# Kernel optimization log

Hardware: AMD Instinct MI355X
Metric: run time of the kernel (lower is better)

The kernel has to match this reference:

```python
import jax, jax.numpy as jnp
import numpy as np

EMBED_DIM = 1024


def setup_inputs() -> dict:
    key = jax.random.key(0)
    ks = jax.random.split(key, 8)
    B, S, D = 4, 2048, EMBED_DIM
    scale = 1.0 / np.sqrt(D)
    x = jax.random.normal(ks[0], (B, S, D), dtype=jnp.float32)
    mask = jnp.zeros((S, S), dtype=jnp.float32)
    # nn.Linear default init ~ U(-1/sqrt(fan_in), 1/sqrt(fan_in)); exact dist irrelevant for correctness
    w_q = jax.random.uniform(ks[1], (D, D), jnp.float32, -scale, scale)
    b_q = jax.random.uniform(ks[2], (D,), jnp.float32, -scale, scale)
    w_k = jax.random.uniform(ks[3], (D, D), jnp.float32, -scale, scale)
    b_k = jax.random.uniform(ks[4], (D,), jnp.float32, -scale, scale)
    w_v = jax.random.uniform(ks[5], (D, D), jnp.float32, -scale, scale)
    b_v = jax.random.uniform(ks[6], (D,), jnp.float32, -scale, scale)
    return {"x": x, "mask": mask, "w_q": w_q, "b_q": b_q,
            "w_k": w_k, "b_k": b_k, "w_v": w_v, "b_v": b_v}


def reference(x, mask, w_q, b_q, w_k, b_k, w_v, b_v):
    D = x.shape[-1]
    # nn.Linear computes x @ W^T + b
    Q = jnp.einsum('bsd,ed->bse', x, w_q) + b_q
    K = jnp.einsum('bsd,ed->bse', x, w_k) + b_k
    V = jnp.einsum('bsd,ed->bse', x, w_v) + b_v
    scores = jnp.einsum('bqd,bkd->bqk', Q, K) / jnp.sqrt(jnp.asarray(D, x.dtype))
    scores = scores + mask  # additive mask, broadcast over batch
    attn = jax.nn.softmax(scores, axis=-1)
    return jnp.einsum('bqk,bkd->bqd', attn, V)
```

## Files before the change

### kernel.cpp

```cpp
#include <hip/hip_runtime.h>


typedef __attribute__((ext_vector_type(8))) short short8;
typedef __attribute__((ext_vector_type(4))) short short4v;
typedef __attribute__((ext_vector_type(4))) float float4v;

__device__ __forceinline__ short f2bf(float f) {
  unsigned u = __builtin_bit_cast(unsigned, f);
  u += 0x7fffu + ((u >> 16) & 1u);
  return (short)(u >> 16);
}
__device__ __forceinline__ float bf2f(short s) {
  unsigned u = ((unsigned)(unsigned short)s) << 16;
  return __builtin_bit_cast(float, u);
}

__device__ __forceinline__ void gl2lds16(const void* g, void* l) {
  __builtin_amdgcn_global_load_lds((const __attribute__((address_space(1))) void*)g,
                                   (__attribute__((address_space(3))) void*)l, 16, 0, 0);
}

__global__ __launch_bounds__(256) void prep_kernel(const float* __restrict__ x,
                                                   const float* __restrict__ wq,
                                                   const float* __restrict__ wk,
                                                   const float* __restrict__ wv,
                                                   const float* __restrict__ bq,
                                                   const float* __restrict__ bk,
                                                   short* __restrict__ x_bf,
                                                   short* __restrict__ w_bf,
                                                   float* __restrict__ bcat) {
  int b = blockIdx.x;
  if (b < 3072) {
    int seg = b >> 10;
    const float* w = seg == 0 ? wq : (seg == 1 ? wk : wv);
    int i = (b - (seg << 10)) * 256 + threadIdx.x;
    float4v v = ((const float4v*)w)[i];
    short4v o;
    o.x = f2bf(v.x); o.y = f2bf(v.y); o.z = f2bf(v.z); o.w = f2bf(v.w);
    ((short4v*)(w_bf + (long)seg * 1048576))[i] = o;
  } else if (b < 11264) {
    int i = (b - 3072) * 256 + threadIdx.x;
    float4v v = ((const float4v*)x)[i];
    short4v o;
    o.x = f2bf(v.x); o.y = f2bf(v.y); o.z = f2bf(v.z); o.w = f2bf(v.w);
    ((short4v*)x_bf)[i] = o;
  } else {
    int i = (b - 11264) * 256 + threadIdx.x;
    if (i < 2048) bcat[i] = i < 1024 ? bq[i] : bk[i - 1024];
  }
}

__device__ __forceinline__ void stage_half(const short* __restrict__ g, int ld,
                                           int grow0, int kt, short* lds, int t) {
  const int r = t >> 3;
  const int cch = (t & 7) ^ (r & 7);
  const long co = (long)kt + cch * 8;
  gl2lds16(g + (long)(grow0 + r) * ld + co, lds + t * 8);
  gl2lds16(g + (long)(grow0 + 64 + r) * ld + co, lds + 4096 + t * 8);
}

template <int EPI, int MH>
__device__ __forceinline__ void gemm_body(const short* __restrict__ A,
                                          const short* __restrict__ Bm,
                                          void* __restrict__ C,
                                          const float* __restrict__ aux,
                                          float* __restrict__ rsum, float scale,
                                          int N, int Kd, int Bld, int m0, int n0,
                                          short (*As)[64], short (*Bs)[64]) {
  const int t = threadIdx.x;
  const int lane = t & 63;
  const int wave = t >> 6;
  const int wm = (wave >> 2) * 64 * MH;
  const int wn = (wave & 3) * 64;
  const int col = lane & 15, quad = lane >> 4;
  const int sw = col & 7;
  const int NT = Kd >> 6;
  constexpr int AS = 128 * MH;

  float4v acc[4 * MH][4] = {};

  stage_half(A, Kd, m0, 0, &As[0][0], t);
  if constexpr (MH == 2) stage_half(A, Kd, m0 + 128, 0, &As[128][0], t);
  stage_half(Bm, Bld, n0, 0, &Bs[0][0], t);
  stage_half(Bm, Bld, n0 + 128, 0, &Bs[128][0], t);
  if (NT > 1) {
    stage_half(A, Kd, m0, 64, &As[AS][0], t);
    if constexpr (MH == 2) stage_half(A, Kd, m0 + 128, 64, &As[AS + 128][0], t);
    stage_half(Bm, Bld, n0, 64, &Bs[256][0], t);
    stage_half(Bm, Bld, n0 + 128, 64, &Bs[384][0], t);
    if constexpr (MH == 2)
      asm volatile("s_waitcnt vmcnt(8)" ::: "memory");
    else
      asm volatile("s_waitcnt vmcnt(6)" ::: "memory");
  } else {
    asm volatile("s_waitcnt vmcnt(0)" ::: "memory");
  }
  __builtin_amdgcn_s_barrier();

  int ar = 0;
  int aw = 2 * AS;
  int br = 0;

  for (int k = 0; k < NT; ++k) {
    short8 a[4][2], b0[2][2], b1[2][2];

    if constexpr (MH == 2) {
#pragma unroll
      for (int i = 0; i < 4; ++i)
#pragma unroll
        for (int s = 0; s < 2; ++s)
          a[i][s] = *(const short8*)&As[ar + wm + i * 16 + col][(((s * 4 + quad) ^ sw)) * 8];
#pragma unroll
      for (int j = 0; j < 2; ++j)
#pragma unroll
        for (int s = 0; s < 2; ++s)
          b0[j][s] = *(const short8*)&Bs[br + wn + j * 16 + col][(((s * 4 + quad) ^ sw)) * 8];
      if (k + 2 < NT) stage_half(A, Kd, m0, (k + 2) * 64, &As[aw][0], t);
      __builtin_amdgcn_s_barrier();
      __builtin_amdgcn_s_setprio(1);
#pragma unroll
      for (int i = 0; i < 4; ++i)
#pragma unroll
        for (int j = 0; j < 2; ++j)
#pragma unroll
          for (int s = 0; s < 2; ++s)
            acc[i][j] = __builtin_amdgcn_mfma_f32_16x16x32_bf16(a[i][s], b0[j][s], acc[i][j], 0, 0, 0);
      __builtin_amdgcn_s_setprio(0);

#pragma unroll
      for (int j = 0; j < 2; ++j)
#pragma unroll
        for (int s = 0; s < 2; ++s)
          b1[j][s] = *(const short8*)&Bs[br + wn + (j + 2) * 16 + col][(((s * 4 + quad) ^ sw)) * 8];
      if (k + 2 < NT) stage_half(A, Kd, m0 + 128, (k + 2) * 64, &As[aw + 128][0], t);
      __builtin_amdgcn_s_barrier();
      __builtin_amdgcn_s_setprio(1);
#pragma unroll
      for (int i = 0; i < 4; ++i)
#pragma unroll
        for (int j = 0; j < 2; ++j)
#pragma unroll
          for (int s = 0; s < 2; ++s)
            acc[i][j + 2] = __builtin_amdgcn_mfma_f32_16x16x32_bf16(a[i][s], b1[j][s], acc[i][j + 2], 0, 0, 0);
      __builtin_amdgcn_s_setprio(0);

#pragma unroll
      for (int i = 0; i < 4; ++i)
#pragma unroll
        for (int s = 0; s < 2; ++s)
          a[i][s] = *(const short8*)&As[ar + wm + (i + 4) * 16 + col][(((s * 4 + quad) ^ sw)) * 8];
      if (k + 2 < NT) stage_half(Bm, Bld, n0, (k + 2) * 64, &Bs[br][0], t);
      __builtin_amdgcn_s_barrier();
      __builtin_amdgcn_s_setprio(1);
#pragma unroll
      for (int i = 0; i < 4; ++i)
#pragma unroll
        for (int j = 0; j < 2; ++j)
#pragma unroll
          for (int s = 0; s < 2; ++s)
            acc[i + 4][j + 2] = __builtin_amdgcn_mfma_f32_16x16x32_bf16(a[i][s], b1[j][s], acc[i + 4][j + 2], 0, 0, 0);
      __builtin_amdgcn_s_setprio(0);

      if (k + 2 < NT) stage_half(Bm, Bld, n0 + 128, (k + 2) * 64, &Bs[br + 128][0], t);
      if (k + 2 < NT) {
        asm volatile("s_waitcnt vmcnt(8)" ::: "memory");
      } else if (k + 1 < NT) {
        asm volatile("s_waitcnt vmcnt(0)" ::: "memory");
      }
      __builtin_amdgcn_s_barrier();
      __builtin_amdgcn_s_setprio(1);
#pragma unroll
      for (int i = 0; i < 4; ++i)
#pragma unroll
        for (int j = 0; j < 2; ++j)
#pragma unroll
          for (int s = 0; s < 2; ++s)
            acc[i + 4][j] = __builtin_amdgcn_mfma_f32_16x16x32_bf16(a[i][s], b0[j][s], acc[i + 4][j], 0, 0, 0);
      __builtin_amdgcn_s_setprio(0);
    } else {
#pragma unroll
      for (int i = 0; i < 4; ++i)
#pragma unroll
        for (int s = 0; s < 2; ++s)
          a[i][s] = *(const short8*)&As[ar + wm + i * 16 + col][(((s * 4 + quad) ^ sw)) * 8];
#pragma unroll
      for (int j = 0; j < 2; ++j)
#pragma unroll
        for (int s = 0; s < 2; ++s)
          b0[j][s] = *(const short8*)&Bs[br + wn + j * 16 + col][(((s * 4 + quad) ^ sw)) * 8];
      if (k + 2 < NT) stage_half(A, Kd, m0, (k + 2) * 64, &As[aw][0], t);
      __builtin_amdgcn_s_barrier();
      __builtin_amdgcn_s_setprio(1);
#pragma unroll
      for (int i = 0; i < 4; ++i)
#pragma unroll
        for (int j = 0; j < 2; ++j)
#pragma unroll
          for (int s = 0; s < 2; ++s)
            acc[i][j] = __builtin_amdgcn_mfma_f32_16x16x32_bf16(a[i][s], b0[j][s], acc[i][j], 0, 0, 0);
      __builtin_amdgcn_s_setprio(0);

#pragma unroll
      for (int j = 0; j < 2; ++j)
#pragma unroll
        for (int s = 0; s < 2; ++s)
          b1[j][s] = *(const short8*)&Bs[br + wn + (j + 2) * 16 + col][(((s * 4 + quad) ^ sw)) * 8];
      if (k + 2 < NT) {
        stage_half(Bm, Bld, n0, (k + 2) * 64, &Bs[br][0], t);
        stage_half(Bm, Bld, n0 + 128, (k + 2) * 64, &Bs[br + 128][0], t);
        asm volatile("s_waitcnt vmcnt(6)" ::: "memory");
      } else if (k + 1 < NT) {
        asm volatile("s_waitcnt vmcnt(0)" ::: "memory");
      }
      __builtin_amdgcn_s_barrier();
      __builtin_amdgcn_s_setprio(1);
#pragma unroll
      for (int i = 0; i < 4; ++i)
#pragma unroll
        for (int j = 0; j < 2; ++j)
#pragma unroll
          for (int s = 0; s < 2; ++s)
            acc[i][j + 2] = __builtin_amdgcn_mfma_f32_16x16x32_bf16(a[i][s], b1[j][s], acc[i][j + 2], 0, 0, 0);
      __builtin_amdgcn_s_setprio(0);
    }

    ar = (ar == 2 * AS) ? 0 : ar + AS;
    aw = (aw == 2 * AS) ? 0 : aw + AS;
    br ^= 256;
  }

  float* invb = (float*)&Bs[0][0];
  if (EPI == 2) {
    __syncthreads();
    if (t < 128 * MH) {
      float s = 0.f;
#pragma unroll
      for (int p = 0; p < 32; ++p) s += aux[p * 8192 + m0 + t];
      invb[t] = __builtin_amdgcn_rcpf(s);
    }
    __syncthreads();
  }

  const float LOG2E = 1.44269504f;
  const float c1 = scale * LOG2E;
#pragma unroll
  for (int i = 0; i < 4 * MH; ++i) {
    float invv[4], addm[4], rsum4[4] = {0.f, 0.f, 0.f, 0.f};
    if (EPI == 2) {
#pragma unroll
      for (int r = 0; r < 4; ++r) invv[r] = invb[wm + i * 16 + quad * 4 + r];
    }
    if (EPI == 3) {
#pragma unroll
      for (int r = 0; r < 4; ++r) addm[r] = aux[m0 + wm + i * 16 + quad * 4 + r];
    }
#pragma unroll
    for (int j = 0; j < 4; ++j) {
      const int n = n0 + wn + j * 16 + col;
      float addn = 0.f;
      if (EPI == 0) addn = aux[n];
#pragma unroll
      for (int r = 0; r < 4; ++r) {
        const int m = m0 + wm + i * 16 + quad * 4 + r;
        float v = acc[i][j][r];
        if (EPI == 0) {
          ((short*)C)[(long)m * N + n] = f2bf(v + addn);
        } else if (EPI == 1) {
          float mv = aux[(long)m * N + n];
          float e = exp2f(fmaf(v, c1, mv * LOG2E));
          short q = f2bf(e);
          ((short*)C)[(long)m * N + n] = q;
          rsum4[r] += bf2f(q);
        } else if (EPI == 2) {
          ((float*)C)[(long)m * N + n] = v * invv[r];
        } else {
          ((short*)C)[(long)m * N + n] = f2bf(v + addm[r]);
        }
      }
    }
    if (EPI == 1) {
#pragma unroll
      for (int r = 0; r < 4; ++r) {
        float s = rsum4[r];
        s += __shfl_xor(s, 1);
        s += __shfl_xor(s, 2);
        s += __shfl_xor(s, 4);
        s += __shfl_xor(s, 8);
        if (col == 0)
          rsum[(wave & 3) * 8192 + m0 + wm + i * 16 + quad * 4 + r] = s;
      }
    }
  }
}

__global__ __launch_bounds__(512, 2) void qkv_kernel(const short* __restrict__ x_bf,
                                                     const short* __restrict__ w_bf,
                                                     short* __restrict__ QK,
                                                     short* __restrict__ Vt,
                                                     const float* __restrict__ bcat,
                                                     const float* __restrict__ bv) {
  __shared__ alignas(16) short As[768][64];
  __shared__ alignas(16) short Bs[512][64];
  const int b = blockIdx.x;
  const int g = (b & 7) * 64 + (b >> 3);
  if (g < 256) {
    const int bz = g >> 7, r = g & 127;
    const int m0 = (r >> 2) * 256, n0 = (r & 3) * 256;
    gemm_body<0, 2>(x_bf, w_bf + (long)bz * 1048576, QK + (long)bz * 8388608,
                    bcat + bz * 1024, nullptr, 1.f, 1024, 1024, 1024, m0, n0, As, Bs);
  } else {
    const int v = g - 256;
    const int m0 = (v >> 5) * 128, n0 = (v & 31) * 256;
    gemm_body<3, 1>(w_bf + 2097152, x_bf, Vt, bv, nullptr, 1.f,
                    8192, 1024, 1024, m0, n0, As, Bs);
  }
}

__global__ __launch_bounds__(512, 2) void scores_kernel(const short* __restrict__ Q,
                                                        const short* __restrict__ Kb,
                                                        short* __restrict__ P,
                                                        const float* __restrict__ mask,
                                                        float* __restrict__ rspart) {
  __shared__ alignas(16) short As[768][64];
  __shared__ alignas(16) short Bs[512][64];
  const int b = blockIdx.x;
  const int g = (b & 7) * 32 + (b >> 3);
  const int bz = g >> 6, t2 = g & 63;
  const int m0 = (t2 >> 3) * 256, n0 = (t2 & 7) * 256;
  gemm_body<1, 2>(Q + (long)bz * 2097152, Kb + (long)bz * 2097152,
                  P + (long)bz * 4194304, mask,
                  rspart + (long)(n0 >> 8) * 4 * 8192 + bz * 2048, 0.03125f,
                  2048, 1024, 1024, m0, n0, As, Bs);
}

__global__ __launch_bounds__(512, 2) void pv_kernel(const short* __restrict__ P,
                                                    const short* __restrict__ Vt,
                                                    float* __restrict__ out,
                                                    const float* __restrict__ rspart) {
  __shared__ alignas(16) short As[384][64];
  __shared__ alignas(16) short Bs[512][64];
  const int b = blockIdx.x;
  const int g = (b & 7) * 32 + (b >> 3);
  const int bz = g >> 6, t2 = g & 63;
  const int m0 = (t2 >> 2) * 128, n0 = (t2 & 3) * 256;
  gemm_body<2, 1>(P + (long)bz * 4194304, Vt + (long)bz * 2048,
                  out + (long)bz * 2097152, rspart + bz * 2048, nullptr, 1.f,
                  1024, 2048, 8192, m0, n0, As, Bs);
}

extern "C" void kernel_launch(void* const* d_in, const int* in_sizes, int n_in,
                              void* d_out, int out_size, void* d_ws, size_t ws_size,
                              hipStream_t stream) {
  const float* x    = (const float*)d_in[0];
  const float* mask = (const float*)d_in[1];
  const float* wq   = (const float*)d_in[2];
  const float* bq   = (const float*)d_in[3];
  const float* wk   = (const float*)d_in[4];
  const float* bk   = (const float*)d_in[5];
  const float* wv   = (const float*)d_in[6];
  const float* bv   = (const float*)d_in[7];
  float* out = (float*)d_out;

  char* ws = (char*)d_ws;
  const size_t MB = 1024 * 1024;
  short* x_bf   = (short*)(ws);
  float* rspart = (float*)(ws);
  short* w_bf   = (short*)(ws + 16 * MB);
  short* QK     = (short*)(ws + 22 * MB);
  short* Vt     = (short*)(ws + 54 * MB);
  short* P      = (short*)(ws + 70 * MB);
  float* bcat   = (float*)(ws + 70 * MB);

  prep_kernel<<<11272, 256, 0, stream>>>(x, wq, wk, wv, bq, bk, x_bf, w_bf, bcat);

  qkv_kernel<<<512, 512, 0, stream>>>(x_bf, w_bf, QK, Vt, bcat, bv);

  short* Q  = QK;
  short* Kb = QK + 8388608;

  scores_kernel<<<256, 512, 0, stream>>>(Q, Kb, P, mask, rspart);

  pv_kernel<<<256, 512, 0, stream>>>(P, Vt, out, rspart);
}
```

Baseline: 255.3 us.

## Use 128x128 tiles with 256-thread blocks for the QKV projection GEMM

Adds a new gemm128 routine with 128x128 output tiles, 4 waves, and a triple-buffered A / double-buffered B LDS pipeline. The QKV kernel now launches 1536 smaller blocks instead of 512 blocks of 256x256 or 128x256 tiles. The aim is better load balance and occupancy across the CUs of the MI355X, since the old launch had few large blocks. In exchange, each output tile reuses less data, so more global and LDS traffic is spent per FLOP.

Result: no change. 259.7 us (+1.7%).

```diff
diff --git a/kernel.cpp b/kernel.cpp
--- a/kernel.cpp
+++ b/kernel.cpp
@@ -59,6 +59,126 @@
   gl2lds16(g + (long)(grow0 + 64 + r) * ld + co, lds + 4096 + t * 8);
 }
 
+__device__ __forceinline__ void stage_tile256(const short* __restrict__ g, int ld,
+                                              int grow0, int kt, short* lds, int t) {
+  const int r0 = t >> 3;
+  const int cch = (t & 7) ^ (r0 & 7);
+  const long co = (long)kt + cch * 8;
+#pragma unroll
+  for (int q = 0; q < 4; ++q)
+    gl2lds16(g + (long)(grow0 + r0 + 32 * q) * ld + co, lds + q * 2048 + t * 8);
+}
+
+template <int EPI>
+__device__ __forceinline__ void gemm128(const short* __restrict__ A,
+                                        const short* __restrict__ Bm,
+                                        void* __restrict__ C,
+                                        const float* __restrict__ aux,
+                                        int N, int Kd, int Bld, int m0, int n0,
+                                        short (*As)[64], short (*Bs)[64]) {
+  const int t = threadIdx.x;
+  const int lane = t & 63;
+  const int wave = t >> 6;
+  const int wm = (wave >> 1) * 64;
+  const int wn = (wave & 1) * 64;
+  const int col = lane & 15, quad = lane >> 4;
+  const int sw = col & 7;
+  const int NT = Kd >> 6;
+
+  float4v acc[4][4] = {};
+
+  stage_tile256(A, Kd, m0, 0, &As[0][0], t);
+  stage_tile256(Bm, Bld, n0, 0, &Bs[0][0], t);
+  if (NT > 1) {
+    stage_tile256(A, Kd, m0, 64, &As[128][0], t);
+    stage_tile256(Bm, Bld, n0, 64, &Bs[128][0], t);
+    asm volatile("s_waitcnt vmcnt(8)" ::: "memory");
+  } else {
+    asm volatile("s_waitcnt vmcnt(0)" ::: "memory");
+  }
+  __builtin_amdgcn_s_barrier();
+
+  int ar = 0, aw = 256, br = 0;
+
+  for (int k = 0; k < NT; ++k) {
+    short8 a[4][2], b0[2][2], b1[2][2];
+
+#pragma unroll
+    for (int i = 0; i < 4; ++i)
+#pragma unroll
+      for (int s = 0; s < 2; ++s)
+        a[i][s] = *(const short8*)&As[ar + wm + i * 16 + col][(((s * 4 + quad) ^ sw)) * 8];
+#pragma unroll
+    for (int j = 0; j < 2; ++j)
+#pragma unroll
+      for (int s = 0; s < 2; ++s)
+        b0[j][s] = *(const short8*)&Bs[br + wn + j * 16 + col][(((s * 4 + quad) ^ sw)) * 8];
+    if (k + 2 < NT) stage_tile256(A, Kd, m0, (k + 2) * 64, &As[aw][0], t);
+    __builtin_amdgcn_s_barrier();
+    __builtin_amdgcn_s_setprio(1);
+#pragma unroll
+    for (int i = 0; i < 4; ++i)
+#pragma unroll
+      for (int j = 0; j < 2; ++j)
+#pragma unroll
+        for (int s = 0; s < 2; ++s)
+          acc[i][j] = __builtin_amdgcn_mfma_f32_16x16x32_bf16(a[i][s], b0[j][s], acc[i][j], 0, 0, 0);
+    __builtin_amdgcn_s_setprio(0);
+
+#pragma unroll
+    for (int j = 0; j < 2; ++j)
+#pragma unroll
+      for (int s = 0; s < 2; ++s)
+        b1[j][s] = *(const short8*)&Bs[br + wn + (j + 2) * 16 + col][(((s * 4 + quad) ^ sw)) * 8];
+    asm volatile("s_waitcnt lgkmcnt(0)" ::: "memory");
+    if (k + 2 < NT) {
+      asm volatile("s_waitcnt vmcnt(4)" ::: "memory");
+    } else if (k + 1 < NT) {
+      asm volatile("s_waitcnt vmcnt(0)" ::: "memory");
+    }
+    __builtin_amdgcn_s_barrier();
+    if (k + 2 < NT) stage_tile256(Bm, Bld, n0, (k + 2) * 64, &Bs[br][0], t);
+    __builtin_amdgcn_s_setprio(1);
+#pragma unroll
+    for (int i = 0; i < 4; ++i)
+#pragma unroll
+      for (int j = 0; j < 2; ++j)
+#pragma unroll
+        for (int s = 0; s < 2; ++s)
+          acc[i][j + 2] = __builtin_amdgcn_mfma_f32_16x16x32_bf16(a[i][s], b1[j][s], acc[i][j + 2], 0, 0, 0);
+    __builtin_amdgcn_s_setprio(0);
+
+    ar = (ar == 256) ? 0 : ar + 128;
+    aw = (aw == 256) ? 0 : aw + 128;
+    br ^= 128;
+  }
+
+#pragma unroll
+  for (int i = 0; i < 4; ++i) {
+    float addm[4];
+    if (EPI == 3) {
+#pragma unroll
+      for (int r = 0; r < 4; ++r) addm[r] = aux[m0 + wm + i * 16 + quad * 4 + r];
+    }
+#pragma unroll
+    for (int j = 0; j < 4; ++j) {
+      const int n = n0 + wn + j * 16 + col;
+      float addn = 0.f;
+      if (EPI == 0) addn = aux[n];
+#pragma unroll
+      for (int r = 0; r < 4; ++r) {
+        const int m = m0 + wm + i * 16 + quad * 4 + r;
+        float v = acc[i][j][r];
+        if (EPI == 0) {
+          ((short*)C)[(long)m * N + n] = f2bf(v + addn);
+        } else {
+          ((short*)C)[(long)m * N + n] = f2bf(v + addm[r]);
+        }
+      }
+    }
+  }
+}
+
 template <int EPI, int MH>
 __device__ __forceinline__ void gemm_body(const short* __restrict__ A,
                                           const short* __restrict__ Bm,
@@ -293,26 +413,24 @@
   }
 }
 
-__global__ __launch_bounds__(512, 2) void qkv_kernel(const short* __restrict__ x_bf,
+__global__ __launch_bounds__(256, 2) void qkv_kernel(const short* __restrict__ x_bf,
                                                      const short* __restrict__ w_bf,
                                                      short* __restrict__ QK,
                                                      short* __restrict__ Vt,
                                                      const float* __restrict__ bcat,
                                                      const float* __restrict__ bv) {
-  __shared__ alignas(16) short As[768][64];
-  __shared__ alignas(16) short Bs[512][64];
+  __shared__ alignas(16) short As[384][64];
+  __shared__ alignas(16) short Bs[256][64];
   const int b = blockIdx.x;
-  const int g = (b & 7) * 64 + (b >> 3);
-  if (g < 256) {
-    const int bz = g >> 7, r = g & 127;
-    const int m0 = (r >> 2) * 256, n0 = (r & 3) * 256;
-    gemm_body<0, 2>(x_bf, w_bf + (long)bz * 1048576, QK + (long)bz * 8388608,
-                    bcat + bz * 1024, nullptr, 1.f, 1024, 1024, 1024, m0, n0, As, Bs);
+  const int g = (b & 7) * 192 + (b >> 3);
+  const int seg = g >> 9, r = g & 511;
+  if (seg < 2) {
+    const int m0 = (r >> 3) * 128, n0 = (r & 7) * 128;
+    gemm128<0>(x_bf, w_bf + (long)seg * 1048576, QK + (long)seg * 8388608,
+               bcat + seg * 1024, 1024, 1024, 1024, m0, n0, As, Bs);
   } else {
-    const int v = g - 256;
-    const int m0 = (v >> 5) * 128, n0 = (v & 31) * 256;
-    gemm_body<3, 1>(w_bf + 2097152, x_bf, Vt, bv, nullptr, 1.f,
-                    8192, 1024, 1024, m0, n0, As, Bs);
+    const int m0 = (r >> 6) * 128, n0 = (r & 63) * 128;
+    gemm128<3>(w_bf + 2097152, x_bf, Vt, bv, 8192, 1024, 1024, m0, n0, As, Bs);
   }
 }
 
@@ -373,7 +491,7 @@
 
   prep_kernel<<<11272, 256, 0, stream>>>(x, wq, wk, wv, bq, bk, x_bf, w_bf, bcat);
 
-  qkv_kernel<<<512, 512, 0, stream>>>(x_bf, w_bf, QK, Vt, bcat, bv);
+  qkv_kernel<<<1536, 256, 0, stream>>>(x_bf, w_bf, QK, Vt, bcat, bv);
 
   short* Q  = QK;
   short* Kb = QK + 8388608;
```
